# Kernel tuning notes

Hardware: AMD Instinct MI355X
Metric: run time of the kernel (lower is better)

Reference implementation:

```python
import jax, jax.numpy as jnp
import numpy as np

B, T = 64, 1024
VOCAB, EMBED, HIDDEN = 55, 64, 128


def setup_inputs() -> dict:
    key = jax.random.key(0)
    ks = jax.random.split(key, 15)
    stdv = 1.0 / np.sqrt(HIDDEN)
    u = lambda k, s: jax.random.uniform(k, s, jnp.float32, -stdv, stdv)
    return {
        "x": jax.random.randint(ks[0], (B, T), 0, VOCAB),
        "emb": jax.random.normal(ks[1], (VOCAB, EMBED), jnp.float32),
        "w_ih0": u(ks[2], (HIDDEN, EMBED)),
        "b_ih0": u(ks[3], (HIDDEN,)),
        "w_hh0": u(ks[4], (HIDDEN, HIDDEN)),
        "b_hh0": u(ks[5], (HIDDEN,)),
        "w_ih1": u(ks[6], (HIDDEN, HIDDEN)),
        "b_ih1": u(ks[7], (HIDDEN,)),
        "w_hh1": u(ks[8], (HIDDEN, HIDDEN)),
        "b_hh1": u(ks[9], (HIDDEN,)),
        "attn_w": u(ks[10], (HIDDEN, HIDDEN)),
        "attn_b": u(ks[11], (HIDDEN,)),
        "fc_w": u(ks[12], (VOCAB, 2 * HIDDEN)),
        "fc_b": u(ks[13], (VOCAB,)),
    }


def reference(x, emb, w_ih0, b_ih0, w_hh0, b_hh0, w_ih1, b_ih1, w_hh1, b_hh1,
              attn_w, attn_b, fc_w, fc_b):
    Bx, Tx = x.shape
    H = w_hh0.shape[0]
    e = emb[x]  # [B, T, E]

    def step(carry, x_t):  # x_t: [B, E]
        h0, h1 = carry
        h0 = jnp.tanh(x_t @ w_ih0.T + b_ih0 + h0 @ w_hh0.T + b_hh0)
        h1 = jnp.tanh(h0 @ w_ih1.T + b_ih1 + h1 @ w_hh1.T + b_hh1)
        return (h0, h1), h1

    init = (jnp.zeros((Bx, H), e.dtype), jnp.zeros((Bx, H), e.dtype))
    _, outs = jax.lax.scan(step, init, jnp.swapaxes(e, 0, 1))  # [T, B, H]
    outs = jnp.swapaxes(outs, 0, 1)  # [B, T, H]

    Q = outs @ attn_w.T + attn_b  # [B, T, H]
    scores = jnp.einsum('bth,bsh->bts', Q, outs) / jnp.sqrt(jnp.asarray(H, e.dtype))
    causal = jnp.tril(jnp.ones((Tx, Tx), bool))  # [T, T]
    scores = jnp.where(causal[None], scores, jnp.asarray(-jnp.inf, scores.dtype))
    attn = jax.nn.softmax(scores, axis=-1)
    context = jnp.einsum('bts,bsh->bth', attn, outs)  # [B, T, H]

    combined = jnp.concatenate([outs, context], axis=-1)  # [B, T, 2H]
    logits = combined @ fc_w.T + fc_b  # [B, T, vocab]
    return logits
```

## Files before the change

### kernel.cpp

```cpp
#include <hip/hip_runtime.h>
#include <hip/hip_bf16.h>
#include <cstdint>
#include <cstddef>


typedef __attribute__((ext_vector_type(8))) short short8;
typedef __attribute__((ext_vector_type(4))) float f32x4;

__device__ __forceinline__ float bf2f(unsigned short u) {
    union { unsigned int i; float f; } c; c.i = ((unsigned int)u) << 16; return c.f;
}
__device__ __forceinline__ unsigned short f2bf(float f) {
    union { float f; unsigned int i; } c; c.f = f;
    unsigned int u = c.i;
    u += 0x7fffu + ((u >> 16) & 1u);
    return (unsigned short)(u >> 16);
}
__device__ __forceinline__ unsigned int pk_bf16(float lo, float hi) {
    union { __hip_bfloat162 h2; unsigned int u; } c;
    c.h2 = __float22bfloat162_rn(make_float2(lo, hi));
    return c.u;
}
__device__ __forceinline__ float fast_tanh(float x) {
    float e = __expf(2.0f * x);
    return 1.0f - 2.0f * __builtin_amdgcn_rcpf(e + 1.0f);
}
__device__ __forceinline__ void bar_lds() {
    asm volatile("s_waitcnt lgkmcnt(0)\n\ts_barrier" ::: "memory");
}
__device__ __forceinline__ short8 ld_a_bf16(const float* p) {
    const float4* q = (const float4*)p;
    float4 f0 = q[0], f1 = q[1];
    short8 r;
    r[0]=(short)f2bf(f0.x); r[1]=(short)f2bf(f0.y);
    r[2]=(short)f2bf(f0.z); r[3]=(short)f2bf(f0.w);
    r[4]=(short)f2bf(f1.x); r[5]=(short)f2bf(f1.y);
    r[6]=(short)f2bf(f1.z); r[7]=(short)f2bf(f1.w);
    return r;
}
__device__ __forceinline__ void ld_fc_hilo(const float* p, short8& hi, short8& lo) {
    const float4* q = (const float4*)p;
    float4 f0 = q[0], f1 = q[1];
    float ff[8] = {f0.x, f0.y, f0.z, f0.w, f1.x, f1.y, f1.z, f1.w};
#pragma unroll
    for (int i = 0; i < 8; ++i) {
        unsigned short hb = f2bf(ff[i]);
        hi[i] = (short)hb;
        lo[i] = (short)f2bf(ff[i] - bf2f(hb));
    }
}

__global__ __launch_bounds__(128)
void k_we(const float* __restrict__ emb, const float* __restrict__ w_ih0,
          const float* __restrict__ b_ih0, const float* __restrict__ b_hh0,
          float* __restrict__ WE)
{
    __shared__ float ev[64];
    const int i = threadIdx.x;
    const int v = blockIdx.x;
    if (i < 64) ev[i] = emb[v * 64 + i];
    __syncthreads();
    float s = b_ih0[i] + b_hh0[i];
    const float* wr = w_ih0 + i * 64;
#pragma unroll
    for (int k = 0; k < 64; ++k) s += wr[k] * ev[k];
    WE[v * 128 + i] = s;
}

__global__ __launch_bounds__(256)
void k_weg(const int* __restrict__ x, const float* __restrict__ WE,
           float* __restrict__ WEg)
{
    __shared__ int xv[32];
    const int tid = threadIdx.x;
    const int b   = blockIdx.y;
    const int t0  = blockIdx.x * 32;
    if (tid < 32) xv[tid] = x[b * 1024 + t0 + tid];
    __syncthreads();
#pragma unroll
    for (int it = 0; it < 4; ++it) {
        int tt = it * 8 + (tid >> 5);
        int c4 = tid & 31;
        float4 v = ((const float4*)(WE + xv[tt] * 128))[c4];
        ((float4*)(WEg + ((size_t)b * 1024 + t0 + tt) * 128))[c4] = v;
    }
}

__global__ __launch_bounds__(512, 1)
void k_scan5(const float* __restrict__ WEg,
             const float* __restrict__ w_hh0,
             const float* __restrict__ w_ih1, const float* __restrict__ b_ih1,
             const float* __restrict__ w_hh1, const float* __restrict__ b_hh1,
             unsigned short* __restrict__ outs_bf)
{
    const int tid   = threadIdx.x;
    const int w     = tid >> 6;
    const int lane  = tid & 63;
    const int quad  = lane >> 4;
    const int n     = lane & 15;
    const int bbase = blockIdx.x * 16;

    __shared__ __align__(16) unsigned short h0buf[2][16][136];
    __shared__ __align__(16) unsigned short h1buf[2][16][136];

    if (w < 4) {
        const int r0 = w * 32 + quad * 4;
        const int r1 = r0 + 16;
        short8 a0[2][4];
#pragma unroll
        for (int r = 0; r < 2; ++r) {
            const size_t mrow = (size_t)(w * 32 + r * 16 + n) * 128;
#pragma unroll
            for (int ks = 0; ks < 4; ++ks)
                a0[r][ks] = ld_a_bf16(w_hh0 + mrow + ks * 32 + quad * 8);
        }
        const size_t wegB0 = (size_t)(bbase + n) * 131072 + r0;
        const size_t wegB1 = wegB0 + 16;
        {
            float4 p0 = *(const float4*)(WEg + wegB0);
            float4 p1 = *(const float4*)(WEg + wegB1);
            *(uint2*)&h0buf[0][n][r0] = make_uint2(
                pk_bf16(fast_tanh(p0.x), fast_tanh(p0.y)),
                pk_bf16(fast_tanh(p0.z), fast_tanh(p0.w)));
            *(uint2*)&h0buf[0][n][r1] = make_uint2(
                pk_bf16(fast_tanh(p1.x), fast_tanh(p1.y)),
                pk_bf16(fast_tanh(p1.z), fast_tanh(p1.w)));
        }
        float4 wA0 = *(const float4*)(WEg + wegB0 + 128);
        float4 wA1 = *(const float4*)(WEg + wegB1 + 128);
        float4 wB0 = *(const float4*)(WEg + wegB0 + 256);
        float4 wB1 = *(const float4*)(WEg + wegB1 + 256);
        float4 wC0 = *(const float4*)(WEg + wegB0 + 384);
        float4 wC1 = *(const float4*)(WEg + wegB1 + 384);
        __syncthreads();

        for (int t = 0; t < 1024; ++t) {
            const int p = t & 1;
            if (t < 1023) {
                const unsigned short* h0p = &h0buf[p][n][quad * 8];
                short8 bh[4];
#pragma unroll
                for (int ks = 0; ks < 4; ++ks)
                    bh[ks] = *(const short8*)(h0p + ks * 32);
                f32x4 c0 = (f32x4){wA0.x, wA0.y, wA0.z, wA0.w};
                f32x4 c1 = (f32x4){wA1.x, wA1.y, wA1.z, wA1.w};
#pragma unroll
                for (int ks = 0; ks < 4; ++ks) {
                    c0 = __builtin_amdgcn_mfma_f32_16x16x32_bf16(a0[0][ks], bh[ks], c0, 0,0,0);
                    c1 = __builtin_amdgcn_mfma_f32_16x16x32_bf16(a0[1][ks], bh[ks], c1, 0,0,0);
                }
                wA0 = wB0; wA1 = wB1; wB0 = wC0; wB1 = wC1;
                const size_t tpre = (size_t)((t + 4 < 1024) ? t + 4 : 1023) * 128;
                wC0 = *(const float4*)(WEg + wegB0 + tpre);
                wC1 = *(const float4*)(WEg + wegB1 + tpre);
                *(uint2*)&h0buf[p ^ 1][n][r0] = make_uint2(
                    pk_bf16(fast_tanh(c0[0]), fast_tanh(c0[1])),
                    pk_bf16(fast_tanh(c0[2]), fast_tanh(c0[3])));
                *(uint2*)&h0buf[p ^ 1][n][r1] = make_uint2(
                    pk_bf16(fast_tanh(c1[0]), fast_tanh(c1[1])),
                    pk_bf16(fast_tanh(c1[2]), fast_tanh(c1[3])));
            }
            bar_lds();
        }
    } else {
        const int w2 = w - 4;
        const int r0 = w2 * 32 + quad * 4;
        const int r1 = r0 + 16;
        short8 a1[2][4], a2[2][4];
#pragma unroll
        for (int r = 0; r < 2; ++r) {
            const size_t mrow = (size_t)(w2 * 32 + r * 16 + n) * 128;
#pragma unroll
            for (int ks = 0; ks < 4; ++ks) {
                a1[r][ks] = ld_a_bf16(w_ih1 + mrow + ks * 32 + quad * 8);
                a2[r][ks] = ld_a_bf16(w_hh1 + mrow + ks * 32 + quad * 8);
            }
        }
        f32x4 b1i[2];
#pragma unroll
        for (int r = 0; r < 2; ++r)
#pragma unroll
            for (int j = 0; j < 4; ++j) {
                int row = w2 * 32 + r * 16 + quad * 4 + j;
                b1i[r][j] = b_ih1[row] + b_hh1[row];
            }
        *(uint2*)&h1buf[0][n][r0] = make_uint2(0u, 0u);
        *(uint2*)&h1buf[0][n][r1] = make_uint2(0u, 0u);
        unsigned short* outp0 = outs_bf + (size_t)(bbase + n) * 131072 + r0;
        unsigned short* outp1 = outp0 + 16;
        __syncthreads();

        for (int t = 0; t < 1024; ++t) {
            const int p = t & 1;
            const unsigned short* h0p = &h0buf[p][n][quad * 8];
            const unsigned short* h1p = &h1buf[p][n][quad * 8];
            short8 bh0[4], bh1[4];
#pragma unroll
            for (int ks = 0; ks < 4; ++ks) {
                bh0[ks] = *(const short8*)(h0p + ks * 32);
                bh1[ks] = *(const short8*)(h1p + ks * 32);
            }
            f32x4 c0 = b1i[0], c1 = b1i[1];
            f32x4 d0 = (f32x4){0.f,0.f,0.f,0.f}, d1 = (f32x4){0.f,0.f,0.f,0.f};
#pragma unroll
            for (int ks = 0; ks < 4; ++ks) {
                c0 = __builtin_amdgcn_mfma_f32_16x16x32_bf16(a1[0][ks], bh0[ks], c0, 0,0,0);
                c1 = __builtin_amdgcn_mfma_f32_16x16x32_bf16(a1[1][ks], bh0[ks], c1, 0,0,0);
                d0 = __builtin_amdgcn_mfma_f32_16x16x32_bf16(a2[0][ks], bh1[ks], d0, 0,0,0);
                d1 = __builtin_amdgcn_mfma_f32_16x16x32_bf16(a2[1][ks], bh1[ks], d1, 0,0,0);
            }
            uint2 o0 = make_uint2(
                pk_bf16(fast_tanh(c0[0] + d0[0]), fast_tanh(c0[1] + d0[1])),
                pk_bf16(fast_tanh(c0[2] + d0[2]), fast_tanh(c0[3] + d0[3])));
            uint2 o1 = make_uint2(
                pk_bf16(fast_tanh(c1[0] + d1[0]), fast_tanh(c1[1] + d1[1])),
                pk_bf16(fast_tanh(c1[2] + d1[2]), fast_tanh(c1[3] + d1[3])));
            *(uint2*)&h1buf[p ^ 1][n][r0] = o0;
            *(uint2*)&h1buf[p ^ 1][n][r1] = o1;
            *(uint2*)(outp0 + (size_t)t * 128) = o0;
            *(uint2*)(outp1 + (size_t)t * 128) = o1;
            bar_lds();
        }
    }
}

__global__ __launch_bounds__(256)
void k_transpose(const unsigned short* __restrict__ outs_bf,
                 unsigned short* __restrict__ outsT)
{
    __shared__ unsigned short lt[128][130];
    const int tid = threadIdx.x;
    const int t0  = blockIdx.x * 128;
    const int b   = blockIdx.y;
    const unsigned int* src =
        (const unsigned int*)(outs_bf + ((size_t)b * 1024 + t0) * 128);
    for (int idx = tid; idx < 8192; idx += 256) {
        int tr = idx >> 6, h2 = idx & 63;
        unsigned int v = src[tr * 64 + h2];
        lt[tr][h2 * 2]     = (unsigned short)(v & 0xffffu);
        lt[tr][h2 * 2 + 1] = (unsigned short)(v >> 16);
    }
    __syncthreads();
    unsigned int* dst = (unsigned int*)(outsT + (size_t)b * 128 * 1024);
    for (int idx = tid; idx < 8192; idx += 256) {
        int h = idx >> 6, t2 = idx & 63;
        unsigned int v = (unsigned int)lt[t2 * 2][h] |
                         ((unsigned int)lt[t2 * 2 + 1][h] << 16);
        dst[h * 512 + (t0 >> 1) + t2] = v;
    }
}

__global__ __launch_bounds__(512, 1)
void k_attnfc(const unsigned short* __restrict__ outs_bf,
              const unsigned short* __restrict__ outsT,
              const float* __restrict__ attn_w, const float* __restrict__ attn_b,
              const float* __restrict__ fc_w, const float* __restrict__ fc_b,
              float* __restrict__ out)
{
    __shared__ __align__(16) unsigned char smem[100352];
    unsigned short* lK = (unsigned short*)smem;
    unsigned short* lV = (unsigned short*)(smem + 32768);
    unsigned short* lP = (unsigned short*)(smem + 65536);

    const int tid  = threadIdx.x;
    const int w    = tid >> 6;
    const int lane = tid & 63;
    const int quad = lane >> 4;
    const int n    = lane & 15;
    const int qt   = blockIdx.x;
    const int b    = blockIdx.y;
    unsigned short* lPw = lP + w * 2176;
    const float cscale = 0.08838834764831845f;

    const unsigned short* outsB = outs_bf + (size_t)b * 131072;
    const int qrow = qt * 128 + w * 16 + n;

    short8 bo[4];
#pragma unroll
    for (int ks = 0; ks < 4; ++ks)
        bo[ks] = *(const short8*)(outsB + (size_t)qrow * 128 + ks * 32 + quad * 8);
#pragma unroll
    for (int mt = 0; mt < 8; ++mt) {
        short8 aw[4];
#pragma unroll
        for (int ks = 0; ks < 4; ++ks)
            aw[ks] = ld_a_bf16(attn_w + (size_t)(mt * 16 + n) * 128 + ks * 32 + quad * 8);
        f32x4 cq;
#pragma unroll
        for (int r = 0; r < 4; ++r) cq[r] = attn_b[mt * 16 + quad * 4 + r];
#pragma unroll
        for (int ks = 0; ks < 4; ++ks)
            cq = __builtin_amdgcn_mfma_f32_16x16x32_bf16(aw[ks], bo[ks], cq, 0,0,0);
        *(uint2*)&lPw[n * 136 + mt * 16 + quad * 4] =
            make_uint2(pk_bf16(cq[0], cq[1]), pk_bf16(cq[2], cq[3]));
    }
    short8 qf[4];
#pragma unroll
    for (int ks = 0; ks < 4; ++ks)
        qf[ks] = *(const short8*)&lPw[n * 136 + ks * 32 + quad * 8];

    f32x4 accO[8];
#pragma unroll
    for (int dt = 0; dt < 8; ++dt) accO[dt] = (f32x4){0.f, 0.f, 0.f, 0.f};
    float mx = -1e30f, lsum = 0.f;

    for (int kt = 0; kt <= qt; ++kt) {
        __syncthreads();
        for (int c = tid; c < 2048; c += 512) {
            int row = c >> 4, k8 = c & 15;
            uint4 vk = *(const uint4*)(outsB + (size_t)(kt * 128 + row) * 128 + k8 * 8);
            *(uint4*)&lK[row * 128 + ((k8 ^ (row & 15)) << 3)] = vk;
            uint4 vv = *(const uint4*)(outsT + ((size_t)b * 128 + row) * 1024 +
                                       kt * 128 + k8 * 8);
            *(uint4*)&lV[row * 128 + ((k8 ^ (row & 15)) << 3)] = vv;
        }
        __syncthreads();
        f32x4 accS[8];
#pragma unroll
        for (int mt = 0; mt < 8; ++mt) {
            short8 af[4];
#pragma unroll
            for (int ks = 0; ks < 4; ++ks) {
                int r = mt * 16 + n;
                af[ks] = *(const short8*)&lK[r * 128 + (((ks * 4 + quad) ^ (r & 15)) << 3)];
            }
            f32x4 s = (f32x4){0.f, 0.f, 0.f, 0.f};
#pragma unroll
            for (int ks = 0; ks < 4; ++ks)
                s = __builtin_amdgcn_mfma_f32_16x16x32_bf16(af[ks], qf[ks], s, 0,0,0);
            accS[mt] = s;
        }
        if (kt == qt) {
            const int ql = w * 16 + n;
#pragma unroll
            for (int mt = 0; mt < 8; ++mt)
#pragma unroll
                for (int jv = 0; jv < 4; ++jv)
                    if (mt * 16 + quad * 4 + jv > ql) accS[mt][jv] = -1e30f;
        }
        float tmax = accS[0][0];
#pragma unroll
        for (int mt = 0; mt < 8; ++mt)
#pragma unroll
            for (int jv = 0; jv < 4; ++jv) tmax = fmaxf(tmax, accS[mt][jv]);
        tmax = fmaxf(tmax, __shfl_xor(tmax, 16));
        tmax = fmaxf(tmax, __shfl_xor(tmax, 32));
        float nm = fmaxf(mx, tmax);
        float alpha = __expf((mx - nm) * cscale);
        float ss = 0.f;
#pragma unroll
        for (int mt = 0; mt < 8; ++mt)
#pragma unroll
            for (int jv = 0; jv < 4; ++jv) {
                float p = __expf((accS[mt][jv] - nm) * cscale);
                accS[mt][jv] = p;
                ss += p;
            }
        ss += __shfl_xor(ss, 16);
        ss += __shfl_xor(ss, 32);
        lsum = lsum * alpha + ss;
        mx = nm;
#pragma unroll
        for (int mt = 0; mt < 8; ++mt)
            *(uint2*)&lPw[n * 136 + mt * 16 + quad * 4] = make_uint2(
                pk_bf16(accS[mt][0], accS[mt][1]),
                pk_bf16(accS[mt][2], accS[mt][3]));
#pragma unroll
        for (int dt = 0; dt < 8; ++dt)
#pragma unroll
            for (int jv = 0; jv < 4; ++jv) accO[dt][jv] *= alpha;
        short8 pf[4];
#pragma unroll
        for (int ks = 0; ks < 4; ++ks)
            pf[ks] = *(const short8*)&lPw[n * 136 + ks * 32 + quad * 8];
#pragma unroll
        for (int dt = 0; dt < 8; ++dt) {
            short8 vf[4];
#pragma unroll
            for (int ks = 0; ks < 4; ++ks) {
                int d = dt * 16 + n;
                vf[ks] = *(const short8*)&lV[d * 128 + (((ks * 4 + quad) ^ (d & 15)) << 3)];
            }
#pragma unroll
            for (int ks = 0; ks < 4; ++ks)
                accO[dt] = __builtin_amdgcn_mfma_f32_16x16x32_bf16(vf[ks], pf[ks], accO[dt], 0,0,0);
        }
    }
    {
        float inv = __builtin_amdgcn_rcpf(lsum);
#pragma unroll
        for (int dt = 0; dt < 8; ++dt)
            *(uint2*)&lPw[n * 136 + dt * 16 + quad * 4] = make_uint2(
                pk_bf16(accO[dt][0] * inv, accO[dt][1] * inv),
                pk_bf16(accO[dt][2] * inv, accO[dt][3] * inv));
    }
    short8 bC[4];
#pragma unroll
    for (int ks = 0; ks < 4; ++ks)
        bC[ks] = *(const short8*)&lPw[n * 136 + ks * 32 + quad * 8];
#pragma unroll
    for (int mt = 0; mt < 4; ++mt) {
        const int vrow = mt * 16 + n;
        f32x4 acc;
#pragma unroll
        for (int r = 0; r < 4; ++r) {
            int vv = mt * 16 + quad * 4 + r;
            acc[r] = (vv < 55) ? fc_b[vv] : 0.f;
        }
#pragma unroll
        for (int c = 0; c < 8; ++c) {
            short8 hi, lo;
            if (vrow < 55) {
                ld_fc_hilo(fc_w + (size_t)vrow * 256 + c * 32 + quad * 8, hi, lo);
            } else {
#pragma unroll
                for (int i = 0; i < 8; ++i) { hi[i] = 0; lo[i] = 0; }
            }
            short8 bb = (c < 4) ? bo[c] : bC[c - 4];
            acc = __builtin_amdgcn_mfma_f32_16x16x32_bf16(hi, bb, acc, 0,0,0);
            acc = __builtin_amdgcn_mfma_f32_16x16x32_bf16(lo, bb, acc, 0,0,0);
        }
#pragma unroll
        for (int r = 0; r < 4; ++r) {
            int vv = mt * 16 + quad * 4 + r;
            if (vv < 55)
                out[((size_t)b * 1024 + qrow) * 55 + vv] = acc[r];
        }
    }
}

extern "C" void kernel_launch(void* const* d_in, const int* in_sizes, int n_in,
                              void* d_out, int out_size, void* d_ws, size_t ws_size,
                              hipStream_t stream)
{
    const int*   x      = (const int*)d_in[0];
    const float* emb    = (const float*)d_in[1];
    const float* w_ih0  = (const float*)d_in[2];
    const float* b_ih0  = (const float*)d_in[3];
    const float* w_hh0  = (const float*)d_in[4];
    const float* b_hh0  = (const float*)d_in[5];
    const float* w_ih1  = (const float*)d_in[6];
    const float* b_ih1  = (const float*)d_in[7];
    const float* w_hh1  = (const float*)d_in[8];
    const float* b_hh1  = (const float*)d_in[9];
    const float* attn_w = (const float*)d_in[10];
    const float* attn_b = (const float*)d_in[11];
    const float* fc_w   = (const float*)d_in[12];
    const float* fc_b   = (const float*)d_in[13];
    float* out = (float*)d_out;

    char* ws = (char*)d_ws;
    unsigned short* outs_bf = (unsigned short*)(ws);
    unsigned short* outsT   = (unsigned short*)(ws + ((size_t)16 << 20));
    float*          WEp     = (float*)         (ws + ((size_t)32 << 20));
    float*          WEg     = (float*)         (ws + ((size_t)33 << 20));

    k_we<<<dim3(55), dim3(128), 0, stream>>>(emb, w_ih0, b_ih0, b_hh0, WEp);
    k_weg<<<dim3(32, 64), dim3(256), 0, stream>>>(x, WEp, WEg);
    k_scan5<<<dim3(4), dim3(512), 0, stream>>>(
        WEg, w_hh0, w_ih1, b_ih1, w_hh1, b_hh1, outs_bf);
    k_transpose<<<dim3(8, 64), dim3(256), 0, stream>>>(outs_bf, outsT);
    k_attnfc<<<dim3(8, 64), dim3(512), 0, stream>>>(
        outs_bf, outsT, attn_w, attn_b, fc_w, fc_b, out);
}
```

Baseline: 791.3 us.

## Prefetch next K/V tile into registers, reverse causal block order, presplit fc weights

The attention kernel now loads the next K/V tile into registers while computing on the current one, so global load latency overlaps the MFMA work. Query tiles are scheduled in reverse order so the longest causal blocks start first, which should reduce tail imbalance. FC weights are split into hi/lo bf16 once by a new small kernel, so each block no longer converts them repeatedly. The cost is extra register pressure from the prefetch buffers and one more kernel launch.

```diff
diff --git a/kernel.cpp b/kernel.cpp
--- a/kernel.cpp
+++ b/kernel.cpp
@@ -38,17 +38,6 @@
     r[6]=(short)f2bf(f1.z); r[7]=(short)f2bf(f1.w);
     return r;
 }
-__device__ __forceinline__ void ld_fc_hilo(const float* p, short8& hi, short8& lo) {
-    const float4* q = (const float4*)p;
-    float4 f0 = q[0], f1 = q[1];
-    float ff[8] = {f0.x, f0.y, f0.z, f0.w, f1.x, f1.y, f1.z, f1.w};
-#pragma unroll
-    for (int i = 0; i < 8; ++i) {
-        unsigned short hb = f2bf(ff[i]);
-        hi[i] = (short)hb;
-        lo[i] = (short)f2bf(ff[i] - bf2f(hb));
-    }
-}
 
 __global__ __launch_bounds__(128)
 void k_we(const float* __restrict__ emb, const float* __restrict__ w_ih0,
@@ -84,6 +73,23 @@
         float4 v = ((const float4*)(WE + xv[tt] * 128))[c4];
         ((float4*)(WEg + ((size_t)b * 1024 + t0 + tt) * 128))[c4] = v;
     }
+}
+
+__global__ __launch_bounds__(256)
+void k_prep(const float* __restrict__ fc_w,
+            unsigned short* __restrict__ fcw_hi,
+            unsigned short* __restrict__ fcw_lo)
+{
+    const int v = blockIdx.x;
+    const int c = threadIdx.x;
+    unsigned short hi = 0, lo = 0;
+    if (v < 55) {
+        float wv = fc_w[v * 256 + c];
+        hi = f2bf(wv);
+        lo = f2bf(wv - bf2f(hi));
+    }
+    fcw_hi[v * 256 + c] = hi;
+    fcw_lo[v * 256 + c] = lo;
 }
 
 __global__ __launch_bounds__(512, 1)
@@ -254,7 +260,9 @@
 void k_attnfc(const unsigned short* __restrict__ outs_bf,
               const unsigned short* __restrict__ outsT,
               const float* __restrict__ attn_w, const float* __restrict__ attn_b,
-              const float* __restrict__ fc_w, const float* __restrict__ fc_b,
+              const unsigned short* __restrict__ fcw_hi,
+              const unsigned short* __restrict__ fcw_lo,
+              const float* __restrict__ fc_b,
               float* __restrict__ out)
 {
     __shared__ __align__(16) unsigned char smem[100352];
@@ -267,13 +275,26 @@
     const int lane = tid & 63;
     const int quad = lane >> 4;
     const int n    = lane & 15;
-    const int qt   = blockIdx.x;
+    const int qt   = 7 - (int)blockIdx.x;
     const int b    = blockIdx.y;
     unsigned short* lPw = lP + w * 2176;
     const float cscale = 0.08838834764831845f;
 
     const unsigned short* outsB = outs_bf + (size_t)b * 131072;
     const int qrow = qt * 128 + w * 16 + n;
+
+    int srow[4], sk8[4];
+#pragma unroll
+    for (int j = 0; j < 4; ++j) {
+        int c = tid + j * 512;
+        srow[j] = c >> 4; sk8[j] = c & 15;
+    }
+    uint4 pk[4], pv[4];
+#pragma unroll
+    for (int j = 0; j < 4; ++j) {
+        pk[j] = *(const uint4*)(outsB + (size_t)(srow[j]) * 128 + sk8[j] * 8);
+        pv[j] = *(const uint4*)(outsT + ((size_t)b * 128 + srow[j]) * 1024 + sk8[j] * 8);
+    }
 
     short8 bo[4];
 #pragma unroll
@@ -306,13 +327,19 @@
 
     for (int kt = 0; kt <= qt; ++kt) {
         __syncthreads();
-        for (int c = tid; c < 2048; c += 512) {
-            int row = c >> 4, k8 = c & 15;
-            uint4 vk = *(const uint4*)(outsB + (size_t)(kt * 128 + row) * 128 + k8 * 8);
-            *(uint4*)&lK[row * 128 + ((k8 ^ (row & 15)) << 3)] = vk;
-            uint4 vv = *(const uint4*)(outsT + ((size_t)b * 128 + row) * 1024 +
-                                       kt * 128 + k8 * 8);
-            *(uint4*)&lV[row * 128 + ((k8 ^ (row & 15)) << 3)] = vv;
+#pragma unroll
+        for (int j = 0; j < 4; ++j) {
+            *(uint4*)&lK[srow[j] * 128 + ((sk8[j] ^ (srow[j] & 15)) << 3)] = pk[j];
+            *(uint4*)&lV[srow[j] * 128 + ((sk8[j] ^ (srow[j] & 15)) << 3)] = pv[j];
+        }
+        if (kt < qt) {
+            const int kn = kt + 1;
+#pragma unroll
+            for (int j = 0; j < 4; ++j) {
+                pk[j] = *(const uint4*)(outsB + (size_t)(kn * 128 + srow[j]) * 128 + sk8[j] * 8);
+                pv[j] = *(const uint4*)(outsT + ((size_t)b * 128 + srow[j]) * 1024 +
+                                        kn * 128 + sk8[j] * 8);
+            }
         }
         __syncthreads();
         f32x4 accS[8];
@@ -409,13 +436,8 @@
         }
 #pragma unroll
         for (int c = 0; c < 8; ++c) {
-            short8 hi, lo;
-            if (vrow < 55) {
-                ld_fc_hilo(fc_w + (size_t)vrow * 256 + c * 32 + quad * 8, hi, lo);
-            } else {
-#pragma unroll
-                for (int i = 0; i < 8; ++i) { hi[i] = 0; lo[i] = 0; }
-            }
+            short8 hi = *(const short8*)(fcw_hi + (size_t)vrow * 256 + c * 32 + quad * 8);
+            short8 lo = *(const short8*)(fcw_lo + (size_t)vrow * 256 + c * 32 + quad * 8);
             short8 bb = (c < 4) ? bo[c] : bC[c - 4];
             acc = __builtin_amdgcn_mfma_f32_16x16x32_bf16(hi, bb, acc, 0,0,0);
             acc = __builtin_amdgcn_mfma_f32_16x16x32_bf16(lo, bb, acc, 0,0,0);
@@ -453,13 +475,16 @@
     unsigned short* outs_bf = (unsigned short*)(ws);
     unsigned short* outsT   = (unsigned short*)(ws + ((size_t)16 << 20));
     float*          WEp     = (float*)         (ws + ((size_t)32 << 20));
+    unsigned short* fcw_hi  = (unsigned short*)(ws + ((size_t)32 << 20) + 65536);
+    unsigned short* fcw_lo  = fcw_hi + 64 * 256;
     float*          WEg     = (float*)         (ws + ((size_t)33 << 20));
 
     k_we<<<dim3(55), dim3(128), 0, stream>>>(emb, w_ih0, b_ih0, b_hh0, WEp);
+    k_prep<<<dim3(64), dim3(256), 0, stream>>>(fc_w, fcw_hi, fcw_lo);
     k_weg<<<dim3(32, 64), dim3(256), 0, stream>>>(x, WEp, WEg);
     k_scan5<<<dim3(4), dim3(512), 0, stream>>>(
         WEg, w_hh0, w_ih1, b_ih1, w_hh1, b_hh1, outs_bf);
     k_transpose<<<dim3(8, 64), dim3(256), 0, stream>>>(outs_bf, outsT);
     k_attnfc<<<dim3(8, 64), dim3(512), 0, stream>>>(
-        outs_bf, outsT, attn_w, attn_b, fc_w, fc_b, out);
-}
+        outs_bf, outsT, attn_w, attn_b, fcw_hi, fcw_lo, fc_b, out);
+}
```

After: 811.4 us. +2.5%, slower.
